# Kernel tuning notes

Measured on AMD Instinct MI355X. Metric: run time of the kernel, lower is better.

## Reference

```python
import jax, jax.numpy as jnp
import numpy as np

MOE_TOPK = 2
NUM_EXPERTS = 8
HIDDEN = 2048
TOKENS = 32768


def setup_inputs() -> dict:
    key = jax.random.key(0)
    k1, k2 = jax.random.split(key)
    x = jax.random.normal(k1, (TOKENS, HIDDEN), dtype=jnp.float32)
    W = jax.random.normal(k2, (NUM_EXPERTS, HIDDEN), dtype=jnp.float32) * 0.02
    return {"x": x, "W": W}


def reference(x, W):
    # gating: [T, H] @ [H, E] -> [T, E]
    logits = jnp.einsum("th,eh->te", x, W)
    # z-loss has no effect on forward values (autograd-side-channel in torch)
    top_logits, top_idx = jax.lax.top_k(logits, MOE_TOPK)  # [T, K]
    scores = jax.nn.softmax(top_logits.astype(jnp.float32), axis=-1).astype(logits.dtype)
    # histogram of expert assignments (torch.histc returns float)
    tokens_per_expert = jnp.zeros((NUM_EXPERTS,), jnp.float32).at[top_idx.reshape(-1)].add(1.0)
    # aux loss also has no effect on forward values
    return scores, top_idx, tokens_per_expert
```

## Files before the change

### kernel.cpp

```cpp
#include <hip/hip_runtime.h>
#include <hip/hip_bf16.h>
#include <math.h>

#define N_TOKENS 32768
#define HIDDEN   2048
#define NEXP     8
#define H4       (HIDDEN / 4)
#define BLOCK    1024
#define WPB      (BLOCK / 64)
#define TOK_PER_WAVE 4
#define GRID     (N_TOKENS / (WPB * TOK_PER_WAVE))

#define SCORES_OFF 0
#define IDX_OFF    (N_TOKENS * 2)
#define HIST_OFF   (N_TOKENS * 4)

__global__ void zero_hist_kernel(float* out) {
    if (threadIdx.x < NEXP) out[HIST_OFF + threadIdx.x] = 0.0f;
}

__device__ __forceinline__ void emit_token(const double* acc, int t,
                                           float* __restrict__ out, unsigned* cnt) {
    double b1 = acc[0]; int i1 = 0;
    double b2 = -1.0e300; int i2 = 0;
#pragma unroll
    for (int e = 1; e < NEXP; ++e) {
        double v = acc[e];
        if (v > b1)      { b2 = b1; i2 = i1; b1 = v; i1 = e; }
        else if (v > b2) { b2 = v;  i2 = e; }
    }
    float d  = (float)(b2 - b1);
    float e1 = expf(d);
    float s0 = 1.0f / (1.0f + e1);

    float2 sc; sc.x = s0; sc.y = e1 * s0;
    float2 ix; ix.x = (float)i1; ix.y = (float)i2;
    *reinterpret_cast<float2*>(out + SCORES_OFF + 2 * t) = sc;
    *reinterpret_cast<float2*>(out + IDX_OFF    + 2 * t) = ix;

    *cnt += (1u << (4 * i1)) + (1u << (4 * i2));
}

__global__ __launch_bounds__(BLOCK, 4) void router_kernel(
        const float* __restrict__ x, const float* __restrict__ W,
        float* __restrict__ out) {
    __shared__ float4 wlds[NEXP * H4];

    const int tid = threadIdx.x;
    const float4* Wv = reinterpret_cast<const float4*>(W);
#pragma unroll
    for (int i = 0; i < (NEXP * H4) / BLOCK; ++i)
        wlds[tid + i * BLOCK] = Wv[tid + i * BLOCK];
    __syncthreads();

    const int wave = tid >> 6;
    const int lane = tid & 63;
    const int gw   = blockIdx.x * WPB + wave;

    unsigned cnt = 0;

#pragma unroll 1
    for (int p = 0; p < TOK_PER_WAVE / 2; ++p) {
        const int t0 = gw * TOK_PER_WAVE + 2 * p;
        const float4* xa = reinterpret_cast<const float4*>(x) + (size_t)t0 * H4;
        const float4* xb = xa + H4;

        double acc[16];
#pragma unroll
        for (int e = 0; e < 16; ++e) acc[e] = 0.0;

#pragma unroll 1
        for (int k = 0; k < 8; k += 2) {
            const float4 a0 = xa[lane + k * 64];
            const float4 a1 = xa[lane + (k + 1) * 64];
            const float4 b0 = xb[lane + k * 64];
            const float4 b1 = xb[lane + (k + 1) * 64];
#pragma unroll
            for (int e = 0; e < NEXP; ++e) {
                const float4 w0 = wlds[e * H4 + lane + k * 64];
                float s0 = w0.x * a0.x;
                s0 = fmaf(w0.y, a0.y, s0); s0 = fmaf(w0.z, a0.z, s0); s0 = fmaf(w0.w, a0.w, s0);
                float s1 = w0.x * b0.x;
                s1 = fmaf(w0.y, b0.y, s1); s1 = fmaf(w0.z, b0.z, s1); s1 = fmaf(w0.w, b0.w, s1);
                const float4 w1 = wlds[e * H4 + lane + (k + 1) * 64];
                s0 = fmaf(w1.x, a1.x, s0); s0 = fmaf(w1.y, a1.y, s0);
                s0 = fmaf(w1.z, a1.z, s0); s0 = fmaf(w1.w, a1.w, s0);
                s1 = fmaf(w1.x, b1.x, s1); s1 = fmaf(w1.y, b1.y, s1);
                s1 = fmaf(w1.z, b1.z, s1); s1 = fmaf(w1.w, b1.w, s1);
                acc[e]     += (double)s0;
                acc[8 + e] += (double)s1;
            }
        }

        {
            const bool u1 = lane & 1;
#pragma unroll
            for (int i = 0; i < 8; ++i) {
                double send = u1 ? acc[i] : acc[8 + i];
                double got  = __shfl_xor(send, 1, 64);
                acc[i] = (u1 ? acc[8 + i] : acc[i]) + got;
            }
            const bool u2 = lane & 2;
#pragma unroll
            for (int i = 0; i < 4; ++i) {
                double send = u2 ? acc[i] : acc[4 + i];
                double got  = __shfl_xor(send, 2, 64);
                acc[i] = (u2 ? acc[4 + i] : acc[i]) + got;
            }
            const bool u4 = lane & 4;
#pragma unroll
            for (int i = 0; i < 2; ++i) {
                double send = u4 ? acc[i] : acc[2 + i];
                double got  = __shfl_xor(send, 4, 64);
                acc[i] = (u4 ? acc[2 + i] : acc[i]) + got;
            }
            const bool u8 = lane & 8;
            {
                double send = u8 ? acc[0] : acc[1];
                double got  = __shfl_xor(send, 8, 64);
                acc[0] = (u8 ? acc[1] : acc[0]) + got;
            }
            acc[0] += __shfl_xor(acc[0], 16, 64);
            acc[0] += __shfl_xor(acc[0], 32, 64);
        }
        double v0[NEXP], v1[NEXP];
#pragma unroll
        for (int e = 0; e < NEXP; ++e) {
            const int r = ((e & 1) << 3) | ((e & 2) << 1) | ((e & 4) >> 1);
            v0[e] = __shfl(acc[0], r,     64);
            v1[e] = __shfl(acc[0], r + 1, 64);
        }
        if (lane == 0) {
            emit_token(v0, t0,     out, &cnt);
            emit_token(v1, t0 + 1, out, &cnt);
        }
    }

    __syncthreads();
    float* h = reinterpret_cast<float*>(wlds);
    if (tid < NEXP) h[tid] = 0.0f;
    __syncthreads();
    if (lane == 0) {
#pragma unroll
        for (int e = 0; e < NEXP; ++e) {
            const unsigned c = (cnt >> (4 * e)) & 0xFu;
            if (c) atomicAdd(&h[e], (float)c);
        }
    }
    __syncthreads();
    if (tid < NEXP) atomicAdd(&out[HIST_OFF + tid], h[tid]);
}

extern "C" void kernel_launch(void* const* d_in, const int* in_sizes, int n_in,
                              void* d_out, int out_size, void* d_ws, size_t ws_size,
                              hipStream_t stream) {
    const float* x = (const float*)d_in[0];
    const float* W = (const float*)d_in[1];
    float* out = (float*)d_out;

    zero_hist_kernel<<<1, 64, 0, stream>>>(out);
    router_kernel<<<GRID, BLOCK, 0, stream>>>(x, W, out);
}
```

Before: 62.44 us.

## Process four tokens per wave per pass with wider butterfly reduction

```diff
diff --git a/kernel.cpp b/kernel.cpp
--- a/kernel.cpp
+++ b/kernel.cpp
@@ -6,10 +6,11 @@
 #define HIDDEN   2048
 #define NEXP     8
 #define H4       (HIDDEN / 4)
-#define BLOCK    1024
+#define BLOCK    512
 #define WPB      (BLOCK / 64)
-#define TOK_PER_WAVE 4
-#define GRID     (N_TOKENS / (WPB * TOK_PER_WAVE))
+#define TPW      4
+#define GROUPS   2
+#define GRID     (N_TOKENS / (WPB * TPW * GROUPS))
 
 #define SCORES_OFF 0
 #define IDX_OFF    (N_TOKENS * 2)
@@ -55,84 +56,102 @@
 
     const int wave = tid >> 6;
     const int lane = tid & 63;
-    const int gw   = blockIdx.x * WPB + wave;
 
     unsigned cnt = 0;
 
 #pragma unroll 1
-    for (int p = 0; p < TOK_PER_WAVE / 2; ++p) {
-        const int t0 = gw * TOK_PER_WAVE + 2 * p;
+    for (int g = 0; g < GROUPS; ++g) {
+        const int t0 = (blockIdx.x * GROUPS + g) * (WPB * TPW) + wave * TPW;
         const float4* xa = reinterpret_cast<const float4*>(x) + (size_t)t0 * H4;
         const float4* xb = xa + H4;
+        const float4* xc = xb + H4;
+        const float4* xd = xc + H4;
 
-        double acc[16];
+        double acc[32];
 #pragma unroll
-        for (int e = 0; e < 16; ++e) acc[e] = 0.0;
+        for (int i = 0; i < 32; ++i) acc[i] = 0.0;
 
 #pragma unroll 1
         for (int k = 0; k < 8; k += 2) {
-            const float4 a0 = xa[lane + k * 64];
-            const float4 a1 = xa[lane + (k + 1) * 64];
-            const float4 b0 = xb[lane + k * 64];
-            const float4 b1 = xb[lane + (k + 1) * 64];
+            const float4 a0 = xa[lane + k * 64], a1 = xa[lane + (k + 1) * 64];
+            const float4 b0 = xb[lane + k * 64], b1 = xb[lane + (k + 1) * 64];
+            const float4 c0 = xc[lane + k * 64], c1 = xc[lane + (k + 1) * 64];
+            const float4 d0 = xd[lane + k * 64], d1 = xd[lane + (k + 1) * 64];
 #pragma unroll
             for (int e = 0; e < NEXP; ++e) {
                 const float4 w0 = wlds[e * H4 + lane + k * 64];
-                float s0 = w0.x * a0.x;
-                s0 = fmaf(w0.y, a0.y, s0); s0 = fmaf(w0.z, a0.z, s0); s0 = fmaf(w0.w, a0.w, s0);
-                float s1 = w0.x * b0.x;
-                s1 = fmaf(w0.y, b0.y, s1); s1 = fmaf(w0.z, b0.z, s1); s1 = fmaf(w0.w, b0.w, s1);
                 const float4 w1 = wlds[e * H4 + lane + (k + 1) * 64];
-                s0 = fmaf(w1.x, a1.x, s0); s0 = fmaf(w1.y, a1.y, s0);
-                s0 = fmaf(w1.z, a1.z, s0); s0 = fmaf(w1.w, a1.w, s0);
-                s1 = fmaf(w1.x, b1.x, s1); s1 = fmaf(w1.y, b1.y, s1);
-                s1 = fmaf(w1.z, b1.z, s1); s1 = fmaf(w1.w, b1.w, s1);
-                acc[e]     += (double)s0;
-                acc[8 + e] += (double)s1;
+                float sa = w0.x * a0.x;
+                sa = fmaf(w0.y, a0.y, sa); sa = fmaf(w0.z, a0.z, sa); sa = fmaf(w0.w, a0.w, sa);
+                sa = fmaf(w1.x, a1.x, sa); sa = fmaf(w1.y, a1.y, sa);
+                sa = fmaf(w1.z, a1.z, sa); sa = fmaf(w1.w, a1.w, sa);
+                float sb = w0.x * b0.x;
+                sb = fmaf(w0.y, b0.y, sb); sb = fmaf(w0.z, b0.z, sb); sb = fmaf(w0.w, b0.w, sb);
+                sb = fmaf(w1.x, b1.x, sb); sb = fmaf(w1.y, b1.y, sb);
+                sb = fmaf(w1.z, b1.z, sb); sb = fmaf(w1.w, b1.w, sb);
+                float sc = w0.x * c0.x;
+                sc = fmaf(w0.y, c0.y, sc); sc = fmaf(w0.z, c0.z, sc); sc = fmaf(w0.w, c0.w, sc);
+                sc = fmaf(w1.x, c1.x, sc); sc = fmaf(w1.y, c1.y, sc);
+                sc = fmaf(w1.z, c1.z, sc); sc = fmaf(w1.w, c1.w, sc);
+                float sd = w0.x * d0.x;
+                sd = fmaf(w0.y, d0.y, sd); sd = fmaf(w0.z, d0.z, sd); sd = fmaf(w0.w, d0.w, sd);
+                sd = fmaf(w1.x, d1.x, sd); sd = fmaf(w1.y, d1.y, sd);
+                sd = fmaf(w1.z, d1.z, sd); sd = fmaf(w1.w, d1.w, sd);
+                acc[e]      += (double)sa;
+                acc[8 + e]  += (double)sb;
+                acc[16 + e] += (double)sc;
+                acc[24 + e] += (double)sd;
             }
         }
 
         {
             const bool u1 = lane & 1;
 #pragma unroll
-            for (int i = 0; i < 8; ++i) {
-                double send = u1 ? acc[i] : acc[8 + i];
+            for (int i = 0; i < 16; ++i) {
+                double send = u1 ? acc[i] : acc[16 + i];
                 double got  = __shfl_xor(send, 1, 64);
-                acc[i] = (u1 ? acc[8 + i] : acc[i]) + got;
+                acc[i] = (u1 ? acc[16 + i] : acc[i]) + got;
             }
             const bool u2 = lane & 2;
 #pragma unroll
-            for (int i = 0; i < 4; ++i) {
-                double send = u2 ? acc[i] : acc[4 + i];
+            for (int i = 0; i < 8; ++i) {
+                double send = u2 ? acc[i] : acc[8 + i];
                 double got  = __shfl_xor(send, 2, 64);
-                acc[i] = (u2 ? acc[4 + i] : acc[i]) + got;
+                acc[i] = (u2 ? acc[8 + i] : acc[i]) + got;
             }
             const bool u4 = lane & 4;
 #pragma unroll
-            for (int i = 0; i < 2; ++i) {
-                double send = u4 ? acc[i] : acc[2 + i];
+            for (int i = 0; i < 4; ++i) {
+                double send = u4 ? acc[i] : acc[4 + i];
                 double got  = __shfl_xor(send, 4, 64);
-                acc[i] = (u4 ? acc[2 + i] : acc[i]) + got;
+                acc[i] = (u4 ? acc[4 + i] : acc[i]) + got;
             }
             const bool u8 = lane & 8;
+#pragma unroll
+            for (int i = 0; i < 2; ++i) {
+                double send = u8 ? acc[i] : acc[2 + i];
+                double got  = __shfl_xor(send, 8, 64);
+                acc[i] = (u8 ? acc[2 + i] : acc[i]) + got;
+            }
+            const bool u16 = lane & 16;
             {
-                double send = u8 ? acc[0] : acc[1];
-                double got  = __shfl_xor(send, 8, 64);
-                acc[0] = (u8 ? acc[1] : acc[0]) + got;
+                double send = u16 ? acc[0] : acc[1];
+                double got  = __shfl_xor(send, 16, 64);
+                acc[0] = (u16 ? acc[1] : acc[0]) + got;
             }
-            acc[0] += __shfl_xor(acc[0], 16, 64);
             acc[0] += __shfl_xor(acc[0], 32, 64);
         }
-        double v0[NEXP], v1[NEXP];
+
 #pragma unroll
-        for (int e = 0; e < NEXP; ++e) {
-            const int r = ((e & 1) << 3) | ((e & 2) << 1) | ((e & 4) >> 1);
-            v0[e] = __shfl(acc[0], r,     64);
-            v1[e] = __shfl(acc[0], r + 1, 64);
-        }
-        if (lane == 0) {
-            emit_token(v0, t0,     out, &cnt);
-            emit_token(v1, t0 + 1, out, &cnt);
+        for (int t = 0; t < TPW; ++t) {
+            double v[NEXP];
+#pragma unroll
+            for (int e = 0; e < NEXP; ++e) {
+                const int r = ((t >> 1) & 1) | ((t & 1) << 1) | (((e >> 2) & 1) << 2)
+                            | (((e >> 1) & 1) << 3) | ((e & 1) << 4);
+                v[e] = __shfl(acc[0], r, 64);
+            }
+            if (lane == 0) emit_token(v, t0 + t, out, &cnt);
         }
     }
 
```

Result: slower. 64.07 us (+2.6%).
